# Kernel tuning notes

Measured on AMD Instinct MI355X. Metric: run time of the kernel, lower is better.

Reference implementation:

```python
import jax, jax.numpy as jnp
import numpy as np

LEVELS = [(128, 128), (64, 64), (32, 32), (16, 16)]  # (H_l, W_l) per feature level
N_TOTAL = sum(h * w for h, w in LEVELS)  # 21760
B, D, H, P, L = 2, 256, 8, 4, 4
HD = D // H
FFN_DIM = 1024


def setup_inputs() -> dict:
    key = jax.random.key(0)
    ks = jax.random.split(key, 12)
    s = 0.02  # weight init scale
    return {
        'embed': jax.random.normal(ks[0], (B, N_TOTAL, D), jnp.float32),
        'pos': jax.random.normal(ks[1], (B, N_TOTAL, D), jnp.float32),
        'ref_points': jax.random.uniform(ks[2], (B, N_TOTAL, L, 2), jnp.float32),
        'ln1_w': jnp.ones((D,), jnp.float32), 'ln1_b': jnp.zeros((D,), jnp.float32),
        'ln2_w': jnp.ones((D,), jnp.float32), 'ln2_b': jnp.zeros((D,), jnp.float32),
        'Wv': jax.random.normal(ks[3], (D, D), jnp.float32) * s, 'bv': jnp.zeros((D,), jnp.float32),
        'Woff': jax.random.normal(ks[4], (D, H * L * P * 2), jnp.float32) * s, 'boff': jnp.zeros((H * L * P * 2,), jnp.float32),
        'Wattn': jax.random.normal(ks[5], (D, H * L * P), jnp.float32) * s, 'battn': jnp.zeros((H * L * P,), jnp.float32),
        'Wo': jax.random.normal(ks[6], (D, D), jnp.float32) * s, 'bo': jnp.zeros((D,), jnp.float32),
        'W1': jax.random.normal(ks[7], (D, FFN_DIM), jnp.float32) * s, 'b1': jnp.zeros((FFN_DIM,), jnp.float32),
        'W2': jax.random.normal(ks[8], (FFN_DIM, D), jnp.float32) * s, 'b2': jnp.zeros((D,), jnp.float32),
        'dimensions': jnp.array(LEVELS, jnp.int32),
    }


def _layer_norm(x, w, b):
    m = jnp.mean(x, axis=-1, keepdims=True)
    v = jnp.mean(jnp.square(x - m), axis=-1, keepdims=True)
    return (x - m) * jax.lax.rsqrt(v + 1e-5) * w + b


def _msda(q, ref, v, dims, Wv, bv, Woff, boff, Wattn, battn, Wo, bo):
    # q, v: (B, N, D); ref: (B, N, L, 2) normalized (x, y)
    Bq, N, _ = q.shape
    value = (v @ Wv + bv).reshape(Bq, N, H, HD)
    off = (q @ Woff + boff).reshape(Bq, N, H, L, P, 2)
    aw = jax.nn.softmax((q @ Wattn + battn).reshape(Bq, N, H, L * P), axis=-1)
    aw = aw.reshape(Bq, N, H, L, P)
    # offset normalizer is [W_l, H_l]
    norm = jnp.stack([dims[:, 1], dims[:, 0]], axis=-1).astype(q.dtype)  # (L, 2)
    loc = ref[:, :, None, :, None, :] + off / norm[None, None, None, :, None, :]  # (B,N,H,L,P,2)

    out = jnp.zeros((Bq, N, H, HD), q.dtype)
    start = 0
    for l, (Hl, Wl) in enumerate(LEVELS):
        S = Hl * Wl
        vl = value[:, start:start + S].transpose(0, 2, 1, 3)  # (B, H, S, hd)
        start += S
        # grid_sample semantics: align_corners=False, zero padding
        x = loc[:, :, :, l, :, 0] * Wl - 0.5  # (B, N, H, P)
        y = loc[:, :, :, l, :, 1] * Hl - 0.5
        x0 = jnp.floor(x); y0 = jnp.floor(y)
        wx = x - x0; wy = y - y0
        x0i = x0.astype(jnp.int32); y0i = y0.astype(jnp.int32)
        samp = jnp.zeros(x.shape + (HD,), q.dtype)
        for dy, dx, w in ((0, 0, (1 - wx) * (1 - wy)), (0, 1, wx * (1 - wy)),
                          (1, 0, (1 - wx) * wy), (1, 1, wx * wy)):
            xi = x0i + dx; yi = y0i + dy
            valid = (xi >= 0) & (xi < Wl) & (yi >= 0) & (yi < Hl)
            idx = jnp.clip(yi, 0, Hl - 1) * Wl + jnp.clip(xi, 0, Wl - 1)  # (B, N, H, P)
            idx_t = idx.transpose(0, 2, 1, 3).reshape(Bq, H, N * P)
            g = jnp.take_along_axis(vl, idx_t[..., None], axis=2)  # (B, H, N*P, hd)
            g = g.reshape(Bq, H, N, P, HD).transpose(0, 2, 1, 3, 4)  # (B, N, H, P, hd)
            samp = samp + (w * valid)[..., None] * g
        out = out + jnp.sum(samp * aw[:, :, :, l, :, None], axis=3)
    return out.reshape(Bq, N, D) @ Wo + bo


def reference(embed, pos, ref_points, ln1_w, ln1_b, ln2_w, ln2_b, Wv, bv, Woff, boff,
              Wattn, battn, Wo, bo, W1, b1, W2, b2, dimensions):
    v = _layer_norm(embed, ln1_w, ln1_b)
    q = v + pos
    embed = embed + _msda(q, ref_points, v, dimensions, Wv, bv, Woff, boff, Wattn, battn, Wo, bo)
    f = _layer_norm(embed, ln2_w, ln2_b)
    embed = embed + jax.nn.relu(f @ W1 + b1) @ W2 + b2
    return embed
```

## Files before the change

### kernel.cpp

```cpp
#include <hip/hip_runtime.h>
#include <cstdint>
#include <cstddef>

#define N_TOTAL 21760
#define BATCH   2
#define M_TOT   (BATCH * N_TOTAL)
#define DMODEL  256
#define NHEAD   8
#define HDIM    32
#define FFN     1024

typedef __bf16 b16x8 __attribute__((ext_vector_type(8)));
typedef float  f32x4 __attribute__((ext_vector_type(4)));

typedef const __attribute__((address_space(1))) void g_void;
typedef __attribute__((address_space(3))) void lds_void;

__device__ __forceinline__ unsigned short f2b(float f) {
  union { float f; unsigned u; } v; v.f = f;
  unsigned r = v.u + 0x7FFF + ((v.u >> 16) & 1);
  return (unsigned short)(r >> 16);
}
__device__ __forceinline__ float b2f(unsigned short u) {
  union { unsigned u; float f; } v; v.u = (unsigned)u << 16;
  return v.f;
}

__global__ void wconv_all(const float* __restrict__ Wv, const float* __restrict__ Woff,
                          const float* __restrict__ Wattn, const float* __restrict__ Wo,
                          const float* __restrict__ W1, const float* __restrict__ W2,
                          unsigned short* __restrict__ dstbase) {
  int idx = blockIdx.x * 256 + threadIdx.x;
  const float* src; int K, N, off;
  if (idx < 65536)       { src = Wv;    K = 256;  N = 256;  off = 0;      }
  else if (idx < 131072) { src = Woff;  K = 256;  N = 256;  off = 65536;  idx -= 65536; }
  else if (idx < 163840) { src = Wattn; K = 256;  N = 128;  off = 131072; idx -= 131072; }
  else if (idx < 229376) { src = Wo;    K = 256;  N = 256;  off = 163840; idx -= 163840; }
  else if (idx < 491520) { src = W1;    K = 256;  N = 1024; off = 229376; idx -= 229376; }
  else if (idx < 753664) { src = W2;    K = 1024; N = 256;  off = 491520; idx -= 491520; }
  else return;
  int k = idx / N, n = idx - k * N;
  dstbase[off + (size_t)n * K + k] = f2b(src[idx]);
}

__global__ void ln1_kernel(const float* __restrict__ x, const float* __restrict__ pos,
                           const float* __restrict__ w, const float* __restrict__ b,
                           unsigned short* __restrict__ vb, unsigned short* __restrict__ qb) {
  int t = threadIdx.x;
  int tkn = blockIdx.x * 4 + (t >> 6);
  int lane = t & 63;
  size_t base = (size_t)tkn * DMODEL + lane * 4;
  float4 xv = *(const float4*)&x[base];
  float s1 = xv.x + xv.y + xv.z + xv.w;
  float s2 = xv.x * xv.x + xv.y * xv.y + xv.z * xv.z + xv.w * xv.w;
  #pragma unroll
  for (int off = 32; off; off >>= 1) {
    s1 += __shfl_down(s1, off);
    s2 += __shfl_down(s2, off);
  }
  s1 = __shfl(s1, 0); s2 = __shfl(s2, 0);
  float m   = s1 * (1.0f / DMODEL);
  float var = s2 * (1.0f / DMODEL) - m * m;
  float rs  = rsqrtf(var + 1e-5f);
  float4 wv = *(const float4*)&w[lane * 4];
  float4 bv = *(const float4*)&b[lane * 4];
  float4 pv = *(const float4*)&pos[base];
  float o0 = (xv.x - m) * rs * wv.x + bv.x;
  float o1 = (xv.y - m) * rs * wv.y + bv.y;
  float o2 = (xv.z - m) * rs * wv.z + bv.z;
  float o3 = (xv.w - m) * rs * wv.w + bv.w;
  ushort4 vo = {f2b(o0), f2b(o1), f2b(o2), f2b(o3)};
  ushort4 qo = {f2b(o0 + pv.x), f2b(o1 + pv.y), f2b(o2 + pv.z), f2b(o3 + pv.w)};
  *(ushort4*)&vb[base] = vo;
  *(ushort4*)&qb[base] = qo;
}

__global__ void ln2_kernel(const float* __restrict__ x, const float* __restrict__ w,
                           const float* __restrict__ b, unsigned short* __restrict__ yb) {
  int t = threadIdx.x;
  int tkn = blockIdx.x * 4 + (t >> 6);
  int lane = t & 63;
  size_t base = (size_t)tkn * DMODEL + lane * 4;
  float4 xv = *(const float4*)&x[base];
  float s1 = xv.x + xv.y + xv.z + xv.w;
  float s2 = xv.x * xv.x + xv.y * xv.y + xv.z * xv.z + xv.w * xv.w;
  #pragma unroll
  for (int off = 32; off; off >>= 1) {
    s1 += __shfl_down(s1, off);
    s2 += __shfl_down(s2, off);
  }
  s1 = __shfl(s1, 0); s2 = __shfl(s2, 0);
  float m   = s1 * (1.0f / DMODEL);
  float var = s2 * (1.0f / DMODEL) - m * m;
  float rs  = rsqrtf(var + 1e-5f);
  float4 wv = *(const float4*)&w[lane * 4];
  float4 bv = *(const float4*)&b[lane * 4];
  ushort4 vo = {f2b((xv.x - m) * rs * wv.x + bv.x), f2b((xv.y - m) * rs * wv.y + bv.y),
                f2b((xv.z - m) * rs * wv.z + bv.z), f2b((xv.w - m) * rs * wv.w + bv.w)};
  *(ushort4*)&yb[base] = vo;
}

__device__ __forceinline__ void gemm_core(
    const unsigned short* __restrict__ A, const unsigned short* __restrict__ Bt,
    const float* __restrict__ bias, const float* __restrict__ addsrc,
    float* __restrict__ Cf, unsigned short* __restrict__ Cb,
    int K, int N, int relu, int row0, int col0,
    unsigned short* As, unsigned short* Bs) {
  int t  = threadIdx.x;
  int w  = t >> 6;
  int l  = t & 63;
  int wm = w >> 1, wn = w & 1;
  int lr = l & 15;
  int kq = l >> 4;

  f32x4 acc[4][4];
  #pragma unroll
  for (int i = 0; i < 4; ++i)
    #pragma unroll
    for (int j = 0; j < 4; ++j) acc[i][j] = (f32x4){0.f, 0.f, 0.f, 0.f};

  int srow = (l >> 3);
  int sseg = (l & 7) * 8;

  for (int k0 = 0; k0 < K; k0 += 64) {
    #pragma unroll
    for (int i = 0; i < 4; ++i) {
      int c = w * 4 + i;
      const unsigned short* ga = A  + (size_t)(row0 + c * 8 + srow) * K + k0 + sseg;
      const unsigned short* gb = Bt + (size_t)(col0 + c * 8 + srow) * K + k0 + sseg;
      __builtin_amdgcn_global_load_lds((g_void*)ga, (lds_void*)(As + c * 512), 16, 0, 0);
      __builtin_amdgcn_global_load_lds((g_void*)gb, (lds_void*)(Bs + c * 512), 16, 0, 0);
    }
    __syncthreads();
    #pragma unroll
    for (int kk = 0; kk < 2; ++kk) {
      b16x8 aF[4], bF[4];
      #pragma unroll
      for (int i = 0; i < 4; ++i)
        aF[i] = *(const b16x8*)&As[(wm * 64 + i * 16 + lr) * 64 + kk * 32 + kq * 8];
      #pragma unroll
      for (int j = 0; j < 4; ++j)
        bF[j] = *(const b16x8*)&Bs[(wn * 64 + j * 16 + lr) * 64 + kk * 32 + kq * 8];
      #pragma unroll
      for (int i = 0; i < 4; ++i)
        #pragma unroll
        for (int j = 0; j < 4; ++j)
          acc[i][j] = __builtin_amdgcn_mfma_f32_16x16x32_bf16(aF[i], bF[j], acc[i][j], 0, 0, 0);
    }
    __syncthreads();
  }

  #pragma unroll
  for (int j = 0; j < 4; ++j) {
    int colg = col0 + wn * 64 + j * 16 + lr;
    float bcol = bias[colg];
    #pragma unroll
    for (int i = 0; i < 4; ++i) {
      int r0g = row0 + wm * 64 + i * 16 + kq * 4;
      #pragma unroll
      for (int r = 0; r < 4; ++r) {
        int rowg = r0g + r;
        float o = acc[i][j][r] + bcol;
        if (relu) o = fmaxf(o, 0.0f);
        if (addsrc) o += addsrc[(size_t)rowg * N + colg];
        if (Cf) Cf[(size_t)rowg * N + colg] = o;
        if (Cb) Cb[(size_t)rowg * N + colg] = f2b(o);
      }
    }
  }
}

__global__ __launch_bounds__(256, 2)
void gemm_bf16(const unsigned short* __restrict__ A,
               const unsigned short* __restrict__ Bt,
               const float* __restrict__ bias, const float* __restrict__ addsrc,
               float* __restrict__ Cf, unsigned short* __restrict__ Cb,
               int K, int N, int relu) {
  __shared__ unsigned short As[128 * 64];
  __shared__ unsigned short Bs[128 * 64];
  gemm_core(A, Bt, bias, addsrc, Cf, Cb, K, N, relu,
            blockIdx.x * 128, blockIdx.y * 128, As, Bs);
}

__global__ __launch_bounds__(256, 2)
void gemm_proj(const unsigned short* __restrict__ vb,
               const unsigned short* __restrict__ qb,
               const unsigned short* __restrict__ Wvt,
               const unsigned short* __restrict__ Wofft,
               const unsigned short* __restrict__ Wattnt,
               const float* __restrict__ bv, const float* __restrict__ boff,
               const float* __restrict__ battn,
               unsigned short* __restrict__ valb,
               unsigned short* __restrict__ offb,
               unsigned short* __restrict__ awb) {
  __shared__ unsigned short As[128 * 64];
  __shared__ unsigned short Bs[128 * 64];
  int y = blockIdx.y;
  const unsigned short* A; const unsigned short* Bt; const float* bias;
  unsigned short* C; int col0, N;
  if (y < 2)      { A = vb; Bt = Wvt;    bias = bv;    C = valb; col0 = y * 128;       N = 256; }
  else if (y < 4) { A = qb; Bt = Wofft;  bias = boff;  C = offb; col0 = (y - 2) * 128; N = 256; }
  else            { A = qb; Bt = Wattnt; bias = battn; C = awb;  col0 = 0;             N = 128; }
  gemm_core(A, Bt, bias, nullptr, nullptr, C, 256, N, 0,
            blockIdx.x * 128, col0, As, Bs);
}

__global__ void msda_kernel(const unsigned short* __restrict__ value,
                            const unsigned short* __restrict__ offb,
                            const unsigned short* __restrict__ awb,
                            const float* __restrict__ ref,
                            unsigned short* __restrict__ outb) {
  __shared__ int2 P[552];
  int tkn = blockIdx.x;
  int t   = threadIdx.x;
  int b   = (tkn >= N_TOTAL) ? 1 : 0;

  if (t < 128) {
    int h = t >> 4, s = t & 15, lev = s >> 2, p = s & 3;
    float lg = b2f(awb[(size_t)tkn * 128 + h * 16 + s]);
    float mx = lg;
    #pragma unroll
    for (int m = 1; m < 16; m <<= 1) mx = fmaxf(mx, __shfl_xor(mx, m, 16));
    float e = __expf(lg - mx);
    float sum = e;
    #pragma unroll
    for (int m = 1; m < 16; m <<= 1) sum += __shfl_xor(sum, m, 16);
    float aw = e / sum;

    const int HL[4] = {128, 64, 32, 16};
    const int ST[4] = {0, 16384, 20480, 21504};
    int Wl = HL[lev];
    float rx = ref[(size_t)tkn * 8 + lev * 2 + 0];
    float ry = ref[(size_t)tkn * 8 + lev * 2 + 1];
    float ox = b2f(offb[(size_t)tkn * 256 + h * 32 + lev * 8 + p * 2 + 0]);
    float oy = b2f(offb[(size_t)tkn * 256 + h * 32 + lev * 8 + p * 2 + 1]);
    float x = rx * (float)Wl + ox - 0.5f;
    float y = ry * (float)Wl + oy - 0.5f;
    float x0f = floorf(x), y0f = floorf(y);
    float wx = x - x0f, wy = y - y0f;
    int x0 = (int)x0f, y0 = (int)y0f;
    float wt[4] = {(1.f - wx) * (1.f - wy), wx * (1.f - wy),
                   (1.f - wx) * wy, wx * wy};
    int base = b * N_TOTAL + ST[lev];
    int pbase = h * 68 + (s >> 2) * 17 + (s & 3) * 4;
    #pragma unroll
    for (int tp = 0; tp < 4; ++tp) {
      int xi = x0 + (tp & 1), yi = y0 + (tp >> 1);
      bool ok = (xi >= 0) & (xi < Wl) & (yi >= 0) & (yi < Wl);
      float wgt = ok ? aw * wt[tp] : 0.f;
      int boff2 = ok ? (((base + yi * Wl + xi) * 256 + h * 32) * 2) : 0;
      P[pbase + tp] = (int2){__float_as_int(wgt), boff2};
    }
  }
  __syncthreads();

  int h = t >> 5, q = (t >> 3) & 3, dq = t & 7;
  int o = h * 68 + q * 17;
  unsigned doff = dq * 8;
  const char* vbase = (const char*)value;
  float a0 = 0.f, a1 = 0.f, a2 = 0.f, a3 = 0.f;
  #pragma unroll 8
  for (int j = 0; j < 16; ++j) {
    int2 pr = P[o + j];
    float wgt = __int_as_float(pr.x);
    unsigned off = (unsigned)pr.y + doff;
    uint2 v = *(const uint2*)(vbase + off);
    union { unsigned u; float f; } l0, h0, l1, h1;
    l0.u = v.x << 16; h0.u = v.x & 0xffff0000u;
    l1.u = v.y << 16; h1.u = v.y & 0xffff0000u;
    a0 += wgt * l0.f; a1 += wgt * h0.f;
    a2 += wgt * l1.f; a3 += wgt * h1.f;
  }
  a0 += __shfl_xor(a0, 8);  a1 += __shfl_xor(a1, 8);
  a2 += __shfl_xor(a2, 8);  a3 += __shfl_xor(a3, 8);
  a0 += __shfl_xor(a0, 16); a1 += __shfl_xor(a1, 16);
  a2 += __shfl_xor(a2, 16); a3 += __shfl_xor(a3, 16);
  if (q == 0) {
    uint2 pk;
    pk.x = (unsigned)f2b(a0) | ((unsigned)f2b(a1) << 16);
    pk.y = (unsigned)f2b(a2) | ((unsigned)f2b(a3) << 16);
    *(uint2*)&outb[(size_t)tkn * 256 + h * 32 + dq * 4] = pk;
  }
}

extern "C" void kernel_launch(void* const* d_in, const int* in_sizes, int n_in,
                              void* d_out, int out_size, void* d_ws, size_t ws_size,
                              hipStream_t stream) {
  const float* embed = (const float*)d_in[0];
  const float* pos   = (const float*)d_in[1];
  const float* refp  = (const float*)d_in[2];
  const float* ln1w  = (const float*)d_in[3];
  const float* ln1b  = (const float*)d_in[4];
  const float* ln2w  = (const float*)d_in[5];
  const float* ln2b  = (const float*)d_in[6];
  const float* Wv    = (const float*)d_in[7];
  const float* bv    = (const float*)d_in[8];
  const float* Woff  = (const float*)d_in[9];
  const float* boff  = (const float*)d_in[10];
  const float* Wattn = (const float*)d_in[11];
  const float* battn = (const float*)d_in[12];
  const float* Wo    = (const float*)d_in[13];
  const float* bo    = (const float*)d_in[14];
  const float* W1    = (const float*)d_in[15];
  const float* b1    = (const float*)d_in[16];
  const float* W2    = (const float*)d_in[17];
  const float* b2    = (const float*)d_in[18];
  float* out = (float*)d_out;
  float* ws  = (float*)d_ws;

  const size_t U = (size_t)M_TOT * DMODEL;
  unsigned short* valb16 = (unsigned short*)ws;
  unsigned short* offb16 = (unsigned short*)(ws + U / 2);
  unsigned short* awb16  = (unsigned short*)(ws + U);
  unsigned short* msdab  = (unsigned short*)(ws + U + U / 4);
  unsigned short* hid16  = (unsigned short*)ws;
  float*          embed2 = ws + 2 * U;
  unsigned short* vb16   = (unsigned short*)(ws + 3 * U);
  unsigned short* qb16   = (unsigned short*)(ws + 3 * U + U / 2);
  unsigned short* fb16   = (unsigned short*)(ws + 4 * U);
  unsigned short* wbuf   = (unsigned short*)(ws + 4 * U + U / 2);

  unsigned short* Wvt    = wbuf;
  unsigned short* Wofft  = wbuf + 65536;
  unsigned short* Wattnt = wbuf + 131072;
  unsigned short* Wot    = wbuf + 163840;
  unsigned short* W1t    = wbuf + 229376;
  unsigned short* W2t    = wbuf + 491520;

  wconv_all<<<(753664 + 255) / 256, 256, 0, stream>>>(Wv, Woff, Wattn, Wo, W1, W2, wbuf);

  ln1_kernel<<<M_TOT / 4, 256, 0, stream>>>(embed, pos, ln1w, ln1b, vb16, qb16);

  gemm_proj<<<dim3(M_TOT / 128, 5), 256, 0, stream>>>(
      vb16, qb16, Wvt, Wofft, Wattnt, bv, boff, battn, valb16, offb16, awb16);

  msda_kernel<<<M_TOT, 256, 0, stream>>>(valb16, offb16, awb16, refp, msdab);

  gemm_bf16<<<dim3(M_TOT / 128, 2), 256, 0, stream>>>(
      msdab, Wot, bo, embed, embed2, nullptr, 256, 256, 0);

  ln2_kernel<<<M_TOT / 4, 256, 0, stream>>>(embed2, ln2w, ln2b, fb16);

  gemm_bf16<<<dim3(M_TOT / 128, 8), 256, 0, stream>>>(
      fb16, W1t, b1, nullptr, nullptr, hid16, 256, 1024, 1);
  gemm_bf16<<<dim3(M_TOT / 128, 2), 256, 0, stream>>>(
      hid16, W2t, b2, embed2, out, nullptr, 1024, 256, 0);
}
```

Before: 348.3 us.

## Store residual in bf16, restructure MSDA gather lanes, raise GEMM occupancy

The intermediate residual embed2 is now stored as bf16 instead of fp32. This halves its write traffic in the Wo GEMM and its reads in ln2 and the W2 GEMM epilogue, at the cost of rounding error in the residual path. The MSDA sampling loop changes to one 4-byte value load per lane over 32 samples, split into two halves with a single shuffle reduction, instead of 8-byte loads over 16 samples with a two-step reduction. The LDS sample table layout is adjusted to match. Launch bounds on the GEMMs go from 2 to 3 blocks per SM, trading register budget for occupancy.

```diff
diff --git a/kernel.cpp b/kernel.cpp
--- a/kernel.cpp
+++ b/kernel.cpp
@@ -75,15 +75,16 @@
   *(ushort4*)&qb[base] = qo;
 }
 
-__global__ void ln2_kernel(const float* __restrict__ x, const float* __restrict__ w,
+__global__ void ln2_kernel(const unsigned short* __restrict__ x, const float* __restrict__ w,
                            const float* __restrict__ b, unsigned short* __restrict__ yb) {
   int t = threadIdx.x;
   int tkn = blockIdx.x * 4 + (t >> 6);
   int lane = t & 63;
   size_t base = (size_t)tkn * DMODEL + lane * 4;
-  float4 xv = *(const float4*)&x[base];
-  float s1 = xv.x + xv.y + xv.z + xv.w;
-  float s2 = xv.x * xv.x + xv.y * xv.y + xv.z * xv.z + xv.w * xv.w;
+  ushort4 xu = *(const ushort4*)&x[base];
+  float x0 = b2f(xu.x), x1 = b2f(xu.y), x2 = b2f(xu.z), x3 = b2f(xu.w);
+  float s1 = x0 + x1 + x2 + x3;
+  float s2 = x0 * x0 + x1 * x1 + x2 * x2 + x3 * x3;
   #pragma unroll
   for (int off = 32; off; off >>= 1) {
     s1 += __shfl_down(s1, off);
@@ -95,14 +96,15 @@
   float rs  = rsqrtf(var + 1e-5f);
   float4 wv = *(const float4*)&w[lane * 4];
   float4 bv = *(const float4*)&b[lane * 4];
-  ushort4 vo = {f2b((xv.x - m) * rs * wv.x + bv.x), f2b((xv.y - m) * rs * wv.y + bv.y),
-                f2b((xv.z - m) * rs * wv.z + bv.z), f2b((xv.w - m) * rs * wv.w + bv.w)};
+  ushort4 vo = {f2b((x0 - m) * rs * wv.x + bv.x), f2b((x1 - m) * rs * wv.y + bv.y),
+                f2b((x2 - m) * rs * wv.z + bv.z), f2b((x3 - m) * rs * wv.w + bv.w)};
   *(ushort4*)&yb[base] = vo;
 }
 
 __device__ __forceinline__ void gemm_core(
     const unsigned short* __restrict__ A, const unsigned short* __restrict__ Bt,
-    const float* __restrict__ bias, const float* __restrict__ addsrc,
+    const float* __restrict__ bias,
+    const float* __restrict__ addf, const unsigned short* __restrict__ addb,
     float* __restrict__ Cf, unsigned short* __restrict__ Cb,
     int K, int N, int relu, int row0, int col0,
     unsigned short* As, unsigned short* Bs) {
@@ -162,7 +164,8 @@
         int rowg = r0g + r;
         float o = acc[i][j][r] + bcol;
         if (relu) o = fmaxf(o, 0.0f);
-        if (addsrc) o += addsrc[(size_t)rowg * N + colg];
+        if (addf) o += addf[(size_t)rowg * N + colg];
+        if (addb) o += b2f(addb[(size_t)rowg * N + colg]);
         if (Cf) Cf[(size_t)rowg * N + colg] = o;
         if (Cb) Cb[(size_t)rowg * N + colg] = f2b(o);
       }
@@ -170,19 +173,20 @@
   }
 }
 
-__global__ __launch_bounds__(256, 2)
+__global__ __launch_bounds__(256, 3)
 void gemm_bf16(const unsigned short* __restrict__ A,
                const unsigned short* __restrict__ Bt,
-               const float* __restrict__ bias, const float* __restrict__ addsrc,
+               const float* __restrict__ bias,
+               const float* __restrict__ addf, const unsigned short* __restrict__ addb,
                float* __restrict__ Cf, unsigned short* __restrict__ Cb,
                int K, int N, int relu) {
   __shared__ unsigned short As[128 * 64];
   __shared__ unsigned short Bs[128 * 64];
-  gemm_core(A, Bt, bias, addsrc, Cf, Cb, K, N, relu,
+  gemm_core(A, Bt, bias, addf, addb, Cf, Cb, K, N, relu,
             blockIdx.x * 128, blockIdx.y * 128, As, Bs);
 }
 
-__global__ __launch_bounds__(256, 2)
+__global__ __launch_bounds__(256, 3)
 void gemm_proj(const unsigned short* __restrict__ vb,
                const unsigned short* __restrict__ qb,
                const unsigned short* __restrict__ Wvt,
@@ -201,7 +205,7 @@
   if (y < 2)      { A = vb; Bt = Wvt;    bias = bv;    C = valb; col0 = y * 128;       N = 256; }
   else if (y < 4) { A = qb; Bt = Wofft;  bias = boff;  C = offb; col0 = (y - 2) * 128; N = 256; }
   else            { A = qb; Bt = Wattnt; bias = battn; C = awb;  col0 = 0;             N = 128; }
-  gemm_core(A, Bt, bias, nullptr, nullptr, C, 256, N, 0,
+  gemm_core(A, Bt, bias, nullptr, nullptr, nullptr, C, 256, N, 0,
             blockIdx.x * 128, col0, As, Bs);
 }
 
@@ -210,7 +214,7 @@
                             const unsigned short* __restrict__ awb,
                             const float* __restrict__ ref,
                             unsigned short* __restrict__ outb) {
-  __shared__ int2 P[552];
+  __shared__ int2 P[544];
   int tkn = blockIdx.x;
   int t   = threadIdx.x;
   int b   = (tkn >= N_TOTAL) ? 1 : 0;
@@ -242,44 +246,40 @@
     float wt[4] = {(1.f - wx) * (1.f - wy), wx * (1.f - wy),
                    (1.f - wx) * wy, wx * wy};
     int base = b * N_TOTAL + ST[lev];
-    int pbase = h * 68 + (s >> 2) * 17 + (s & 3) * 4;
     #pragma unroll
     for (int tp = 0; tp < 4; ++tp) {
+      int e4 = s * 4 + tp;
+      int idx = h * 68 + (e4 >> 5) * 34 + (e4 & 31);
       int xi = x0 + (tp & 1), yi = y0 + (tp >> 1);
       bool ok = (xi >= 0) & (xi < Wl) & (yi >= 0) & (yi < Wl);
       float wgt = ok ? aw * wt[tp] : 0.f;
       int boff2 = ok ? (((base + yi * Wl + xi) * 256 + h * 32) * 2) : 0;
-      P[pbase + tp] = (int2){__float_as_int(wgt), boff2};
+      P[idx] = (int2){__float_as_int(wgt), boff2};
     }
   }
   __syncthreads();
 
-  int h = t >> 5, q = (t >> 3) & 3, dq = t & 7;
-  int o = h * 68 + q * 17;
-  unsigned doff = dq * 8;
+  int h = t >> 5, g = t & 31, dp = g & 15, half = g >> 4;
+  int o = h * 68 + half * 34;
+  unsigned doff = dp * 4;
   const char* vbase = (const char*)value;
-  float a0 = 0.f, a1 = 0.f, a2 = 0.f, a3 = 0.f;
+  float accL = 0.f, accH = 0.f;
   #pragma unroll 8
-  for (int j = 0; j < 16; ++j) {
+  for (int j = 0; j < 32; ++j) {
     int2 pr = P[o + j];
     float wgt = __int_as_float(pr.x);
-    unsigned off = (unsigned)pr.y + doff;
-    uint2 v = *(const uint2*)(vbase + off);
-    union { unsigned u; float f; } l0, h0, l1, h1;
-    l0.u = v.x << 16; h0.u = v.x & 0xffff0000u;
-    l1.u = v.y << 16; h1.u = v.y & 0xffff0000u;
-    a0 += wgt * l0.f; a1 += wgt * h0.f;
-    a2 += wgt * l1.f; a3 += wgt * h1.f;
-  }
-  a0 += __shfl_xor(a0, 8);  a1 += __shfl_xor(a1, 8);
-  a2 += __shfl_xor(a2, 8);  a3 += __shfl_xor(a3, 8);
-  a0 += __shfl_xor(a0, 16); a1 += __shfl_xor(a1, 16);
-  a2 += __shfl_xor(a2, 16); a3 += __shfl_xor(a3, 16);
-  if (q == 0) {
-    uint2 pk;
-    pk.x = (unsigned)f2b(a0) | ((unsigned)f2b(a1) << 16);
-    pk.y = (unsigned)f2b(a2) | ((unsigned)f2b(a3) << 16);
-    *(uint2*)&outb[(size_t)tkn * 256 + h * 32 + dq * 4] = pk;
+    unsigned v = *(const unsigned*)(vbase + (size_t)((unsigned)pr.y + doff));
+    union { unsigned u; float f; } lo, hi;
+    lo.u = v << 16;
+    hi.u = v & 0xffff0000u;
+    accL += wgt * lo.f;
+    accH += wgt * hi.f;
+  }
+  accL += __shfl_xor(accL, 16);
+  accH += __shfl_xor(accH, 16);
+  if (half == 0) {
+    unsigned pk = (unsigned)f2b(accL) | ((unsigned)f2b(accH) << 16);
+    *(unsigned*)&outb[(size_t)tkn * 256 + h * 32 + dp * 2] = pk;
   }
 }
 
@@ -314,7 +314,7 @@
   unsigned short* awb16  = (unsigned short*)(ws + U);
   unsigned short* msdab  = (unsigned short*)(ws + U + U / 4);
   unsigned short* hid16  = (unsigned short*)ws;
-  float*          embed2 = ws + 2 * U;
+  unsigned short* emb2b  = (unsigned short*)(ws + 2 * U);
   unsigned short* vb16   = (unsigned short*)(ws + 3 * U);
   unsigned short* qb16   = (unsigned short*)(ws + 3 * U + U / 2);
   unsigned short* fb16   = (unsigned short*)(ws + 4 * U);
@@ -337,12 +337,12 @@
   msda_kernel<<<M_TOT, 256, 0, stream>>>(valb16, offb16, awb16, refp, msdab);
 
   gemm_bf16<<<dim3(M_TOT / 128, 2), 256, 0, stream>>>(
-      msdab, Wot, bo, embed, embed2, nullptr, 256, 256, 0);
-
-  ln2_kernel<<<M_TOT / 4, 256, 0, stream>>>(embed2, ln2w, ln2b, fb16);
+      msdab, Wot, bo, embed, nullptr, nullptr, emb2b, 256, 256, 0);
+
+  ln2_kernel<<<M_TOT / 4, 256, 0, stream>>>(emb2b, ln2w, ln2b, fb16);
 
   gemm_bf16<<<dim3(M_TOT / 128, 8), 256, 0, stream>>>(
-      fb16, W1t, b1, nullptr, nullptr, hid16, 256, 1024, 1);
+      fb16, W1t, b1, nullptr, nullptr, nullptr, hid16, 256, 1024, 1);
   gemm_bf16<<<dim3(M_TOT / 128, 2), 256, 0, stream>>>(
-      hid16, W2t, b2, embed2, out, nullptr, 1024, 256, 0);
-}
+      hid16, W2t, b2, nullptr, emb2b, out, nullptr, 1024, 256, 0);
+}
```

Result: faster. 316.0 us (-9.3%).
